# Kernel optimization log

Hardware: AMD Instinct MI355X
Metric: run time of the kernel (lower is better)

Reference implementation:

```python
import jax, jax.numpy as jnp
import numpy as np

VOCAB, D = 32000, 128
B, R, C, T = 8, 100, 64, 32


def setup_inputs() -> dict:
    key = jax.random.key(0)
    k1, k2, k3 = jax.random.split(key, 3)
    x = jax.random.randint(k1, (B, R, C, T), 0, VOCAB, dtype=jnp.int32)
    W_embed = jax.random.normal(k2, (VOCAB, D), dtype=jnp.float32)
    w_pred = jax.random.normal(k3, (1, D), dtype=jnp.float32) * (1.0 / np.sqrt(D))
    b_pred = jnp.zeros((1,), dtype=jnp.float32)
    return {"x": x, "W_embed": W_embed, "w_pred": w_pred, "b_pred": b_pred}


def reference(x, W_embed, w_pred, b_pred):
    # Embedding gather for every cell token at once: [B,R,C,T,D]
    emb = W_embed[x]
    # Mean over tokens within each cell: [B,R,C,D]
    pooled = emb.mean(axis=-2)
    # Dropout is identity in eval mode. Exact (erf) GELU as in torch nn.GELU default.
    act = jax.nn.gelu(pooled, approximate=False)
    # Linear(D -> 1), squeeze to scalar per cell: [B,R,C]
    out = jnp.einsum('brcd,d->brc', act, w_pred[0]) + b_pred[0]
    return out
```

## Files before the change

kernel.cpp:

```cpp
#include <hip/hip_runtime.h>
#include <hip/hip_bf16.h>
#include <math.h>
#include <string.h>

constexpr int VOCAB  = 32000;
constexpr int D      = 128;
constexpr int T      = 32;
constexpr int NCELLS = 8 * 100 * 64;
constexpr int NCHUNK = 2;
constexpr int CDIM   = D / NCHUNK;
constexpr int CHUNK_ELEMS2 = VOCAB * (CDIM / 2);

__device__ inline ushort f2bf(float f) {
    uint32_t u;
    memcpy(&u, &f, 4);
    u += 0x7FFFu + ((u >> 16) & 1u);
    return (ushort)(u >> 16);
}

__device__ inline float gelu_fast(float xv) {
    const float is2 = 0.70710678118654752440f;
    float y  = xv * is2;
    float av = fabsf(y);
    float t  = __builtin_amdgcn_rcpf(__builtin_fmaf(0.3275911f, av, 1.0f));
    float p  = 0.254829592f + t * (-0.284496736f + t * (1.421413741f
             + t * (-1.453152027f + t * 1.061405429f)));
    float e  = __expf(-av * av);
    float er = 1.0f - p * t * e;
    er = copysignf(er, y);
    return 0.5f * xv * (1.0f + er);
}

__global__ __launch_bounds__(256) void convert_W_kernel(
    const float* __restrict__ W, ushort* __restrict__ Wb, float* __restrict__ out)
{
    const int i = blockIdx.x * blockDim.x + threadIdx.x;
    const int v = i >> 5;
    const int k = i & 31;
    const int chunk = k >> 4;
    const int sub   = k & 15;

    float4 src = reinterpret_cast<const float4*>(W)[i];
    ushort4 o;
    o.x = f2bf(src.x); o.y = f2bf(src.y); o.z = f2bf(src.z); o.w = f2bf(src.w);
    reinterpret_cast<ushort4*>(Wb)[(size_t)chunk * (VOCAB * 16) + (size_t)v * 16 + sub] = o;

    if (i < NCELLS) out[i] = 0.0f;
}

__global__ __launch_bounds__(256) void gather_kernel(
    const int*    __restrict__ x,
    const ushort* __restrict__ Wb,
    const float*  __restrict__ w_pred,
    const float*  __restrict__ b_pred,
    float*        __restrict__ out)
{
    const int wave = threadIdx.x >> 6;
    const int lane = threadIdx.x & 63;

    const int slot  = blockIdx.x & 7;
    const int chunk = slot >> 2;
    const int sub   = slot & 3;
    const int g     = blockIdx.x >> 3;
    const int cell  = ((g << 2) + sub) * 4 + wave;

    const int j    = lane & 31;
    const int half = lane >> 5;

    int myidx  = __builtin_nontemporal_load(x + (size_t)cell * T + j);
    int rowoff = myidx << 5;

    const __hip_bfloat162* __restrict__ tbl =
        reinterpret_cast<const __hip_bfloat162*>(Wb) + (size_t)chunk * CHUNK_ELEMS2;

    float ax = 0.0f, ay = 0.0f;
    #pragma unroll
    for (int i = 0; i < T / 2; ++i) {
        int e = __shfl(rowoff, 2 * i + half, 64);
        __hip_bfloat162 v = tbl[(uint32_t)(e + j)];
        float2 f = __bfloat1622float2(v);
        ax += f.x;
        ay += f.y;
    }
    ax += __shfl_xor(ax, 32, 64);
    ay += __shfl_xor(ay, 32, 64);

    float p = (half ? ay : ax) * (1.0f / (float)T);
    float gl = gelu_fast(p);
    float wv = w_pred[chunk * CDIM + 2 * j + half];
    float s = gl * wv;

    #pragma unroll
    for (int off = 32; off >= 1; off >>= 1)
        s += __shfl_xor(s, off, 64);

    if (lane == 0) {
        if (chunk == 0) s += b_pred[0];
        atomicAdd(&out[cell], s);
    }
}

extern "C" void kernel_launch(void* const* d_in, const int* in_sizes, int n_in,
                              void* d_out, int out_size, void* d_ws, size_t ws_size,
                              hipStream_t stream) {
    const int*   x      = (const int*)  d_in[0];
    const float* W      = (const float*)d_in[1];
    const float* w_pred = (const float*)d_in[2];
    const float* b_pred = (const float*)d_in[3];
    float*       out    = (float*)d_out;
    ushort*      Wb     = (ushort*)d_ws;

    const int conv_groups = VOCAB * D / 4;
    convert_W_kernel<<<conv_groups / 256, 256, 0, stream>>>(W, Wb, out);

    gather_kernel<<<NCHUNK * (NCELLS / 4), 256, 0, stream>>>(x, Wb, w_pred, b_pred, out);
}
```

Baseline: 106.2 us.

## Gather 8-byte bf16 row slices per lane with vector token loads and prescaled table

The gather is reorganized so each lane reads 8 tokens via two 16-byte index loads and fetches 8-byte (4 bf16) slices of each row, instead of shuffling token offsets and loading 4 bytes per lane per step. Partial sums are reduced across lane quarters with xor shuffles, and the 1/T mean scale is folded into the bf16 conversion of the table. This aims to cut the number of load instructions and shuffles per cell. It adds extra reduction shuffles, and prescaling before rounding to bf16 slightly changes numerics.

```diff
diff --git a/kernel.cpp b/kernel.cpp
--- a/kernel.cpp
+++ b/kernel.cpp
@@ -1,5 +1,4 @@
 #include <hip/hip_runtime.h>
-#include <hip/hip_bf16.h>
 #include <math.h>
 #include <string.h>
 
@@ -9,13 +8,21 @@
 constexpr int NCELLS = 8 * 100 * 64;
 constexpr int NCHUNK = 2;
 constexpr int CDIM   = D / NCHUNK;
-constexpr int CHUNK_ELEMS2 = VOCAB * (CDIM / 2);
+constexpr int ROWB   = CDIM * 2;
+
+typedef int   v4i __attribute__((ext_vector_type(4)));
+typedef float v2f __attribute__((ext_vector_type(2)));
 
 __device__ inline ushort f2bf(float f) {
     uint32_t u;
     memcpy(&u, &f, 4);
     u += 0x7FFFu + ((u >> 16) & 1u);
     return (ushort)(u >> 16);
+}
+__device__ inline float hi16f(uint32_t b) {
+    float f;
+    memcpy(&f, &b, 4);
+    return f;
 }
 
 __device__ inline float gelu_fast(float xv) {
@@ -40,9 +47,11 @@
     const int chunk = k >> 4;
     const int sub   = k & 15;
 
+    const float sc = 1.0f / (float)T;
     float4 src = reinterpret_cast<const float4*>(W)[i];
     ushort4 o;
-    o.x = f2bf(src.x); o.y = f2bf(src.y); o.z = f2bf(src.z); o.w = f2bf(src.w);
+    o.x = f2bf(src.x * sc); o.y = f2bf(src.y * sc);
+    o.z = f2bf(src.z * sc); o.w = f2bf(src.w * sc);
     reinterpret_cast<ushort4*>(Wb)[(size_t)chunk * (VOCAB * 16) + (size_t)v * 16 + sub] = o;
 
     if (i < NCELLS) out[i] = 0.0f;
@@ -64,35 +73,54 @@
     const int g     = blockIdx.x >> 3;
     const int cell  = ((g << 2) + sub) * 4 + wave;
 
-    const int j    = lane & 31;
-    const int half = lane >> 5;
+    const int q = lane >> 4;
+    const int h = lane & 15;
 
-    int myidx  = __builtin_nontemporal_load(x + (size_t)cell * T + j);
-    int rowoff = myidx << 5;
+    const v4i* xq = reinterpret_cast<const v4i*>(x + ((size_t)cell << 5)) + (q << 1);
+    v4i ta = __builtin_nontemporal_load(xq);
+    v4i tb = __builtin_nontemporal_load(xq + 1);
+    int tok[8] = {ta.x, ta.y, ta.z, ta.w, tb.x, tb.y, tb.z, tb.w};
 
-    const __hip_bfloat162* __restrict__ tbl =
-        reinterpret_cast<const __hip_bfloat162*>(Wb) + (size_t)chunk * CHUNK_ELEMS2;
+    const char* __restrict__ base =
+        reinterpret_cast<const char*>(Wb) + (size_t)chunk * (VOCAB * ROWB);
+    const uint32_t h8 = (uint32_t)(h << 3);
 
-    float ax = 0.0f, ay = 0.0f;
+    uint2 u[8];
     #pragma unroll
-    for (int i = 0; i < T / 2; ++i) {
-        int e = __shfl(rowoff, 2 * i + half, 64);
-        __hip_bfloat162 v = tbl[(uint32_t)(e + j)];
-        float2 f = __bfloat1622float2(v);
-        ax += f.x;
-        ay += f.y;
+    for (int i = 0; i < 8; ++i) {
+        uint32_t ob = ((uint32_t)tok[i] << 7) + h8;
+        u[i] = *reinterpret_cast<const uint2*>(base + ob);
     }
-    ax += __shfl_xor(ax, 32, 64);
-    ay += __shfl_xor(ay, 32, 64);
 
-    float p = (half ? ay : ax) * (1.0f / (float)T);
-    float gl = gelu_fast(p);
-    float wv = w_pred[chunk * CDIM + 2 * j + half];
-    float s = gl * wv;
+    v2f A = {0.f, 0.f}, B = {0.f, 0.f};
+    #pragma unroll
+    for (int i = 0; i < 8; ++i) {
+        v2f fa = {hi16f(u[i].x << 16), hi16f(u[i].x & 0xffff0000u)};
+        v2f fb = {hi16f(u[i].y << 16), hi16f(u[i].y & 0xffff0000u)};
+        A += fa;
+        B += fb;
+    }
+
+    A.x += __shfl_xor(A.x, 16, 64);
+    A.y += __shfl_xor(A.y, 16, 64);
+    B.x += __shfl_xor(B.x, 16, 64);
+    B.y += __shfl_xor(B.y, 16, 64);
+    A.x += __shfl_xor(A.x, 32, 64);
+    A.y += __shfl_xor(A.y, 32, 64);
+    B.x += __shfl_xor(B.x, 32, 64);
+    B.y += __shfl_xor(B.y, 32, 64);
+
+    float v01 = (q & 1) ? A.y : A.x;
+    float v23 = (q & 1) ? B.y : B.x;
+    float pv  = (q & 2) ? v23 : v01;
+
+    float gl = gelu_fast(pv);
+    float wv = w_pred[chunk * CDIM + (h << 2) + q];
+    float s  = gl * wv;
 
     #pragma unroll
-    for (int off = 32; off >= 1; off >>= 1)
-        s += __shfl_xor(s, off, 64);
+    for (int o = 32; o >= 1; o >>= 1)
+        s += __shfl_xor(s, o, 64);
 
     if (lane == 0) {
         if (chunk == 0) s += b_pred[0];
```

New measurement: 115.0 us. 8.3% more time.
